# Kernel tuning notes

Hardware: AMD Instinct MI355X
Metric: run time of the kernel (lower is better)

The kernel has to match this reference:

```python
import jax, jax.numpy as jnp
import numpy as np

N_NODES = 100000
N_EDGES = 3200000
IN_CH = 512
HID_CH = 40   # 2 * out_channels
OUT_CH = 20


def setup_inputs() -> dict:
    key = jax.random.key(0)
    k1, k2, k3, k4, k5, k6 = jax.random.split(key, 6)
    x = jax.random.normal(k1, (N_NODES, IN_CH), dtype=jnp.float32)
    edge_index = jax.random.randint(k2, (2, N_EDGES), 0, N_NODES, dtype=jnp.int32)
    # Glorot-style init for GCN weights, zero bias (PyG default)
    W1 = jax.random.normal(k3, (IN_CH, HID_CH), dtype=jnp.float32) * (1.0 / np.sqrt(IN_CH))
    b1 = jnp.zeros((HID_CH,), dtype=jnp.float32)
    W2 = jax.random.normal(k4, (HID_CH, OUT_CH), dtype=jnp.float32) * (1.0 / np.sqrt(HID_CH))
    b2 = jnp.zeros((OUT_CH,), dtype=jnp.float32)
    return {"x": x, "edge_index": edge_index, "W1": W1, "b1": b1, "W2": W2, "b2": b2}


def _gcn_conv(x, src, dst, W, b):
    """PyG GCNConv: add self-loops, symmetric norm, linear, scatter-add, bias."""
    n = x.shape[0]
    loops = jnp.arange(n, dtype=src.dtype)
    src = jnp.concatenate([src, loops])
    dst = jnp.concatenate([dst, loops])
    # in-degree over A + I (self-loops guarantee deg >= 1)
    deg = jax.ops.segment_sum(jnp.ones(src.shape[0], x.dtype), dst, num_segments=n)
    dinv = jax.lax.rsqrt(deg)
    norm = dinv[src] * dinv[dst]               # [E+N]
    h = x @ W                                   # [N, out] GEMM before aggregation
    msg = h[src] * norm[:, None]                # gather + scale
    out = jax.ops.segment_sum(msg, dst, num_segments=n)  # scatter-add at targets
    return out + b


def reference(x, edge_index, W1, b1, W2, b2):
    src, dst = edge_index[0], edge_index[1]
    h = jax.nn.relu(_gcn_conv(x, src, dst, W1, b1))
    # dropout is identity in eval mode (training=False)
    return _gcn_conv(h, src, dst, W2, b2)
```

## Files before the change

### kernel.cpp

```cpp
#include <hip/hip_runtime.h>
#include <cstddef>

static constexpr int NN   = 100000;
static constexpr int NE   = 3200000;
static constexpr int CIN  = 512;
static constexpr int CHID = 40;
static constexpr int COUT = 20;


__global__ __launch_bounds__(256) void k_count(const int* __restrict__ dst, int* __restrict__ cnt,
                                               int* __restrict__ rank, int n_edges) {
  const int e = blockIdx.x * 256 + threadIdx.x;
  if (e < n_edges) rank[e] = atomicAdd(&cnt[dst[e]], 1);
}

__global__ __launch_bounds__(256) void k_scanA(const int* __restrict__ cnt, int* __restrict__ excl,
                                               int* __restrict__ bsums, float* __restrict__ dinv, int n) {
  __shared__ int sdata[256];
  const int t = threadIdx.x;
  const int base = blockIdx.x * 1024 + t * 4;
  int v[4];
#pragma unroll
  for (int j = 0; j < 4; ++j) {
    const int i = base + j;
    v[j] = (i < n) ? cnt[i] : 0;
    if (i < n) dinv[i] = rsqrtf((float)(v[j] + 1));
  }
  const int s4 = v[0] + v[1] + v[2] + v[3];
  sdata[t] = s4;
  __syncthreads();
  for (int off = 1; off < 256; off <<= 1) {
    int val = 0;
    if (t >= off) val = sdata[t - off];
    __syncthreads();
    sdata[t] += val;
    __syncthreads();
  }
  int run = sdata[t] - s4;
#pragma unroll
  for (int j = 0; j < 4; ++j) {
    const int i = base + j;
    if (i < n) excl[i] = run;
    run += v[j];
  }
  if (t == 255) bsums[blockIdx.x] = sdata[255];
}

__global__ __launch_bounds__(256) void k_scanB(int* __restrict__ bsums, int nb) {
  __shared__ int sdata[256];
  const int t = threadIdx.x;
  const int v = (t < nb) ? bsums[t] : 0;
  sdata[t] = v;
  __syncthreads();
  for (int off = 1; off < 256; off <<= 1) {
    int val = 0;
    if (t >= off) val = sdata[t - off];
    __syncthreads();
    sdata[t] += val;
    __syncthreads();
  }
  if (t < nb) bsums[t] = sdata[t] - v;
}

__global__ __launch_bounds__(256) void k_scanC(int* __restrict__ rowptr, const int* __restrict__ boff,
                                               int n, int n_edges) {
  const int i = blockIdx.x * 256 + threadIdx.x;
  if (i < n) rowptr[i] += boff[i >> 10];
  if (i == 0) rowptr[n] = n_edges;
}

__global__ __launch_bounds__(256) void k_fill(const int* __restrict__ src, const int* __restrict__ dst,
                                              const int* __restrict__ rank, const int* __restrict__ rowptr,
                                              int* __restrict__ csr_src, int n_edges) {
  const int e = blockIdx.x * 256 + threadIdx.x;
  if (e >= n_edges) return;
  const int d = dst[e];
  const int pos = rowptr[d] + rank[e];
  csr_src[pos] = src[e];
}


__global__ __launch_bounds__(256) void k_gemm1(const float* __restrict__ x, const float* __restrict__ W,
                                               float* __restrict__ h, int n) {
  const int node = blockIdx.x * 256 + threadIdx.x;
  if (node >= n) return;
  const float4* __restrict__ x4 = (const float4*)(x + (size_t)node * CIN);
  float acc[CHID];
#pragma unroll
  for (int c = 0; c < CHID; ++c) acc[c] = 0.f;
  for (int kk = 0; kk < CIN / 4; ++kk) {
    const float4 xv = x4[kk];
    const float* __restrict__ Wk = W + kk * 4 * CHID;
#pragma unroll
    for (int c = 0; c < CHID; ++c) {
      float a = acc[c];
      a = fmaf(xv.x, Wk[c], a);
      a = fmaf(xv.y, Wk[CHID + c], a);
      a = fmaf(xv.z, Wk[2 * CHID + c], a);
      a = fmaf(xv.w, Wk[3 * CHID + c], a);
      acc[c] = a;
    }
  }
  float* __restrict__ o = h + (size_t)node * CHID;
#pragma unroll
  for (int c = 0; c < CHID; ++c) o[c] = acc[c];
}

__global__ __launch_bounds__(256) void k_gemm2(const float* __restrict__ t1, const float* __restrict__ W,
                                               float* __restrict__ g, int n) {
  const int node = blockIdx.x * 256 + threadIdx.x;
  if (node >= n) return;
  const float4* __restrict__ r4 = (const float4*)(t1 + (size_t)node * CHID);
  float acc[COUT];
#pragma unroll
  for (int c = 0; c < COUT; ++c) acc[c] = 0.f;
#pragma unroll
  for (int kk = 0; kk < CHID / 4; ++kk) {
    const float4 xv = r4[kk];
    const float* __restrict__ Wk = W + kk * 4 * COUT;
#pragma unroll
    for (int c = 0; c < COUT; ++c) {
      float a = acc[c];
      a = fmaf(xv.x, Wk[c], a);
      a = fmaf(xv.y, Wk[COUT + c], a);
      a = fmaf(xv.z, Wk[2 * COUT + c], a);
      a = fmaf(xv.w, Wk[3 * COUT + c], a);
      acc[c] = a;
    }
  }
  float* __restrict__ o = g + (size_t)node * COUT;
#pragma unroll
  for (int c = 0; c < COUT; ++c) o[c] = acc[c];
}

__global__ __launch_bounds__(256) void k_agg40(const float* __restrict__ h, const int* __restrict__ rowptr,
                                               const int* __restrict__ csr_src, const float* __restrict__ dinv,
                                               const float* __restrict__ bias, float* __restrict__ out, int n) {
  const int wid = (blockIdx.x * 256 + (int)threadIdx.x) >> 6;
  const int lane = threadIdx.x & 63;
  if (wid >= n) return;
  const int node = __builtin_amdgcn_readfirstlane(wid);
  const int r0 = rowptr[node];
  const int r1 = rowptr[node + 1];
  const float dv = dinv[node];
  const float self_w = dv * dv;
  const bool act = lane < CHID;
  float acc = 0.f;
  if (act) acc = h[(size_t)node * CHID + lane] * self_w;
  int i = r0;
  for (; i + 4 <= r1; i += 4) {
    const int s0 = csr_src[i + 0];
    const int s1 = csr_src[i + 1];
    const int s2 = csr_src[i + 2];
    const int s3 = csr_src[i + 3];
    const float w0 = dinv[s0] * dv;
    const float w1 = dinv[s1] * dv;
    const float w2 = dinv[s2] * dv;
    const float w3 = dinv[s3] * dv;
    if (act) {
      const float g0 = h[(size_t)s0 * CHID + lane];
      const float g1 = h[(size_t)s1 * CHID + lane];
      const float g2 = h[(size_t)s2 * CHID + lane];
      const float g3 = h[(size_t)s3 * CHID + lane];
      acc = fmaf(g0, w0, acc);
      acc = fmaf(g1, w1, acc);
      acc = fmaf(g2, w2, acc);
      acc = fmaf(g3, w3, acc);
    }
  }
  for (; i < r1; ++i) {
    const int s = csr_src[i];
    const float w = dinv[s] * dv;
    if (act) acc = fmaf(h[(size_t)s * CHID + lane], w, acc);
  }
  if (act) {
    float v = acc + bias[lane];
    v = fmaxf(v, 0.f);
    out[(size_t)node * CHID + lane] = v;
  }
}

__global__ __launch_bounds__(256) void k_agg20(const float* __restrict__ h, const int* __restrict__ rowptr,
                                               const int* __restrict__ csr_src, const float* __restrict__ dinv,
                                               const float* __restrict__ bias, float* __restrict__ out, int n) {
  const int wave = (blockIdx.x * 256 + (int)threadIdx.x) >> 6;
  const int lane = threadIdx.x & 63;
  const int sub = lane / COUT;
  const int ch = lane % COUT;
  const int node = wave * 3 + sub;
  if (sub >= 3 || node >= n) return;
  const int r0 = rowptr[node];
  const int r1 = rowptr[node + 1];
  const float dv = dinv[node];
  float acc = h[(size_t)node * COUT + ch] * (dv * dv);
  int i = r0;
  for (; i + 2 <= r1; i += 2) {
    const int s0 = csr_src[i + 0];
    const int s1 = csr_src[i + 1];
    const float w0 = dinv[s0] * dv;
    const float w1 = dinv[s1] * dv;
    acc = fmaf(h[(size_t)s0 * COUT + ch], w0, acc);
    acc = fmaf(h[(size_t)s1 * COUT + ch], w1, acc);
  }
  if (i < r1) {
    const int s = csr_src[i];
    acc = fmaf(h[(size_t)s * COUT + ch], dinv[s] * dv, acc);
  }
  out[(size_t)node * COUT + ch] = acc + bias[ch];
}


extern "C" void kernel_launch(void* const* d_in, const int* in_sizes, int n_in,
                              void* d_out, int out_size, void* d_ws, size_t ws_size,
                              hipStream_t stream) {
  const float* x   = (const float*)d_in[0];
  const int*   ei  = (const int*)d_in[1];
  const float* W1  = (const float*)d_in[2];
  const float* b1  = (const float*)d_in[3];
  const float* W2  = (const float*)d_in[4];
  const float* b2  = (const float*)d_in[5];
  float* out = (float*)d_out;

  const int* srcp = ei;
  const int* dstp = ei + NE;

  char* ws = (char*)d_ws;
  size_t off = 0;
  auto take = [&](size_t bytes) -> char* {
    char* p = ws + off;
    off = (off + bytes + 255) & ~(size_t)255;
    return p;
  };
  int*   cnt     = (int*)take((size_t)NN * 4);
  int*   rowptr  = (int*)take((size_t)(NN + 1) * 4);
  float* dinv    = (float*)take((size_t)NN * 4);
  int*   bsums   = (int*)take(256 * 4);
  int*   rank    = (int*)take((size_t)NE * 4);
  int*   csr_src = (int*)take((size_t)NE * 4);
  float* h1      = (float*)take((size_t)NN * CHID * 4);
  float* t1      = (float*)take((size_t)NN * CHID * 4);
  float* g2      = h1;

  (void)in_sizes; (void)n_in; (void)out_size; (void)ws_size;

  hipMemsetAsync(cnt, 0, (size_t)NN * 4, stream);

  k_count<<<(NE + 255) / 256, 256, 0, stream>>>(dstp, cnt, rank, NE);
  const int nb = (NN + 1023) / 1024;
  k_scanA<<<nb, 256, 0, stream>>>(cnt, rowptr, bsums, dinv, NN);
  k_scanB<<<1, 256, 0, stream>>>(bsums, nb);
  k_scanC<<<(NN + 255) / 256, 256, 0, stream>>>(rowptr, bsums, NN, NE);
  k_fill<<<(NE + 255) / 256, 256, 0, stream>>>(srcp, dstp, rank, rowptr, csr_src, NE);

  k_gemm1<<<(NN + 255) / 256, 256, 0, stream>>>(x, W1, h1, NN);
  k_agg40<<<(NN + 3) / 4, 256, 0, stream>>>(h1, rowptr, csr_src, dinv, b1, t1, NN);
  k_gemm2<<<(NN + 255) / 256, 256, 0, stream>>>(t1, W2, g2, NN);
  const int nwaves2 = (NN + 2) / 3;
  k_agg20<<<(nwaves2 + 3) / 4, 256, 0, stream>>>(g2, rowptr, csr_src, dinv, b2, out, NN);
}
```

Baseline: 832.4 us.

## Restructure first-layer GEMM to stage x tiles in LDS and split output channels

Each block now handles 64 nodes, with four waves each computing 10 of the 40 output channels. The waves cooperatively load 128-column chunks of x into a padded LDS tile, then read their node's row from LDS. The old kernel had one thread per node, each streaming a 2KB row and holding 40 accumulators. The new layout is meant to reduce register pressure and raise occupancy, while keeping weight reads wave-uniform and broadcast. The cost is LDS traffic and two barriers per chunk.

```diff
diff --git a/kernel.cpp b/kernel.cpp
--- a/kernel.cpp
+++ b/kernel.cpp
@@ -79,31 +79,71 @@
   csr_src[pos] = src[e];
 }
 
-
 __global__ __launch_bounds__(256) void k_gemm1(const float* __restrict__ x, const float* __restrict__ W,
                                                float* __restrict__ h, int n) {
-  const int node = blockIdx.x * 256 + threadIdx.x;
-  if (node >= n) return;
-  const float4* __restrict__ x4 = (const float4*)(x + (size_t)node * CIN);
-  float acc[CHID];
-#pragma unroll
-  for (int c = 0; c < CHID; ++c) acc[c] = 0.f;
-  for (int kk = 0; kk < CIN / 4; ++kk) {
-    const float4 xv = x4[kk];
-    const float* __restrict__ Wk = W + kk * 4 * CHID;
-#pragma unroll
-    for (int c = 0; c < CHID; ++c) {
-      float a = acc[c];
-      a = fmaf(xv.x, Wk[c], a);
-      a = fmaf(xv.y, Wk[CHID + c], a);
-      a = fmaf(xv.z, Wk[2 * CHID + c], a);
-      a = fmaf(xv.w, Wk[3 * CHID + c], a);
-      acc[c] = a;
-    }
-  }
-  float* __restrict__ o = h + (size_t)node * CHID;
-#pragma unroll
-  for (int c = 0; c < CHID; ++c) o[c] = acc[c];
+  __shared__ float tile[64 * 129];
+  const int t = threadIdx.x;
+  const int nl = t & 63;
+  const int cg = __builtin_amdgcn_readfirstlane(t >> 6);
+  const int node0 = blockIdx.x * 64;
+  const int node = node0 + nl;
+  const bool nok = node < n;
+
+  float acc[10];
+#pragma unroll
+  for (int c = 0; c < 10; ++c) acc[c] = 0.f;
+
+  const float4* __restrict__ xs = (const float4*)(x + (size_t)node * CIN);
+
+  for (int chunk = 0; chunk < 4; ++chunk) {
+    float4 v[8];
+    if (nok) {
+#pragma unroll
+      for (int j = 0; j < 8; ++j) v[j] = xs[chunk * 32 + cg * 8 + j];
+    } else {
+#pragma unroll
+      for (int j = 0; j < 8; ++j) v[j] = make_float4(0.f, 0.f, 0.f, 0.f);
+    }
+    __syncthreads();
+    float* __restrict__ wp = &tile[nl * 129 + cg * 32];
+#pragma unroll
+    for (int j = 0; j < 8; ++j) {
+      wp[j * 4 + 0] = v[j].x;
+      wp[j * 4 + 1] = v[j].y;
+      wp[j * 4 + 2] = v[j].z;
+      wp[j * 4 + 3] = v[j].w;
+    }
+    __syncthreads();
+
+    const float* __restrict__ Wc = W + (size_t)chunk * 128 * CHID + cg * 10;
+    const float* __restrict__ xr = &tile[nl * 129];
+#pragma unroll 4
+    for (int k = 0; k < 128; k += 4) {
+      const float x0 = xr[k + 0];
+      const float x1 = xr[k + 1];
+      const float x2 = xr[k + 2];
+      const float x3 = xr[k + 3];
+      const float* __restrict__ w0 = Wc + (size_t)(k + 0) * CHID;
+      const float* __restrict__ w1 = Wc + (size_t)(k + 1) * CHID;
+      const float* __restrict__ w2 = Wc + (size_t)(k + 2) * CHID;
+      const float* __restrict__ w3 = Wc + (size_t)(k + 3) * CHID;
+#pragma unroll
+      for (int c = 0; c < 10; ++c) {
+        float a = acc[c];
+        a = fmaf(x0, w0[c], a);
+        a = fmaf(x1, w1[c], a);
+        a = fmaf(x2, w2[c], a);
+        a = fmaf(x3, w3[c], a);
+        acc[c] = a;
+      }
+    }
+  }
+
+  if (nok) {
+    float* __restrict__ o = h + (size_t)node * CHID + cg * 10;
+#pragma unroll
+    for (int c = 0; c < 10; ++c) o[c] = acc[c];
+  }
 }
 
 __global__ __launch_bounds__(256) void k_gemm2(const float* __restrict__ t1, const float* __restrict__ W,
@@ -252,7 +292,7 @@
   k_scanC<<<(NN + 255) / 256, 256, 0, stream>>>(rowptr, bsums, NN, NE);
   k_fill<<<(NE + 255) / 256, 256, 0, stream>>>(srcp, dstp, rank, rowptr, csr_src, NE);
 
-  k_gemm1<<<(NN + 255) / 256, 256, 0, stream>>>(x, W1, h1, NN);
+  k_gemm1<<<(NN + 63) / 64, 256, 0, stream>>>(x, W1, h1, NN);
   k_agg40<<<(NN + 3) / 4, 256, 0, stream>>>(h1, rowptr, csr_src, dinv, b1, t1, NN);
   k_gemm2<<<(NN + 255) / 256, 256, 0, stream>>>(t1, W2, g2, NN);
   const int nwaves2 = (NN + 2) / 3;
```

Measured after the change: 838.6 us. Within noise of the previous version (+0.7%).
